# Optimization experiments

Hardware: AMD Instinct MI355X
Metric: run time of the kernel (lower is better)

The kernel has to match this reference:

```python
import jax, jax.numpy as jnp
import numpy as np

R = 8  # patch radius (init kwarg)


def setup_inputs() -> dict:
    key = jax.random.key(0)
    k1, k2, k3 = jax.random.split(key, 3)
    B, H, W, N = 8, 1024, 1024, 4096
    image1 = jax.random.normal(k1, (B, 1, H, W), dtype=jnp.float32)
    image2 = jax.random.normal(k2, (B, 1, H, W), dtype=jnp.float32)
    # (x1, y1, x2, y2) integer pixel coords in [0, H-1]
    matches = jax.random.randint(k3, (B, N, 4), 0, H, dtype=jnp.int32)
    return {"image1": image1, "image2": image2, "matches": matches}


def _normalize(p):
    # per-patch zero-mean / unit-std (unbiased std, matching torch.std)
    m = p.mean(axis=-1, keepdims=True)
    s = p.std(axis=-1, keepdims=True, ddof=1)
    return (p - m) / (s + 1e-4)


def reference(image1, image2, matches):
    r = R
    d = 2 * r + 1
    # offset grid, flattened row-major: lines[i,j]=i, columns[i,j]=j
    lines = jnp.repeat(jnp.arange(d, dtype=jnp.int32), d)   # [d^2]
    cols = jnp.tile(jnp.arange(d, dtype=jnp.int32), d)      # [d^2]
    # original M = [lines, columns, lines, columns]
    off = jnp.stack([lines, cols, lines, cols], axis=0)      # [4, d^2]
    idx = matches[..., None].astype(jnp.int32) + off          # [B, N, 4, d^2]

    def pad(im):  # [B,1,H,W] -> [B, H+2r, W+2r]
        return jnp.pad(im[:, 0], ((0, 0), (r, r), (r, r)))

    img1p, img2p = pad(image1), pad(image2)
    b = jnp.arange(matches.shape[0])[:, None, None]           # [B,1,1]
    # rows come from y-coord columns (1,3), cols from x-coord columns (0,2)
    p1 = img1p[b, idx[:, :, 1, :], idx[:, :, 0, :]]           # [B, N, d^2]
    p2 = img2p[b, idx[:, :, 3, :], idx[:, :, 2, :]]           # [B, N, d^2]
    return jnp.concatenate([_normalize(p1), _normalize(p2)], axis=-1)  # [B, N, 2*d^2]
```

## Files before the change

kernel.cpp:

```cpp
#include <hip/hip_runtime.h>
#include <hip/hip_bf16.h>


#define IMG_H 1024
#define IMG_W 1024
#define NMATCH 4096
#define DPATCH 17
#define NPATCH 289
#define RAD 8

__global__ __launch_bounds__(256) void prewarm_kernel(
    const float* __restrict__ img1,
    const float* __restrict__ img2)
{
    const int tid = blockIdx.x * blockDim.x + threadIdx.x;
    const int nthreads = gridDim.x * blockDim.x;
    const float4* __restrict__ a = (const float4*)img1;
    const float4* __restrict__ b = (const float4*)img2;
    const int n4 = (8 * IMG_H * IMG_W) / 4;
    float s = 0.f;
    for (int i = tid; i < n4; i += nthreads) {
        float4 x = a[i];
        float4 y = b[i];
        s += x.x + x.y + x.z + x.w + y.x + y.y + y.z + y.w;
    }
    asm volatile("" :: "v"(s));
}

__global__ __launch_bounds__(256) void extract_patch_kernel(
    const float* __restrict__ img1,
    const float* __restrict__ img2,
    const int* __restrict__ matches,
    float* __restrict__ out)
{
    __shared__ float smem[4 * NPATCH];

    const int tid  = blockIdx.x * blockDim.x + threadIdx.x;
    const int wave = tid >> 6;
    const int lane = tid & 63;
    const int pair  = wave >> 1;
    const int which = wave & 1;
    const int wbase = (threadIdx.x >> 6) * NPATCH;

    const int* m = matches + pair * 4;
    const int mx = m[which ? 2 : 0];
    const int my = m[which ? 3 : 1];

    const int b = pair >> 12;
    const float* __restrict__ imgb =
        (which ? img2 : img1) + (size_t)b * (IMG_H * IMG_W);

    const int g = lane / DPATCH;
    const int c = lane - g * DPATCH;
    const int ix = mx + c - RAD;
    const bool col_ok = (g < 3) && ((unsigned)ix < IMG_W);

    float sum = 0.f, sumsq = 0.f;
#pragma unroll
    for (int it = 0; it < 6; ++it) {
        const int r = it * 3 + g;
        float val = 0.f;
        if (g < 3 && r < DPATCH) {
            const int iy = my + r - RAD;
            if (col_ok && (unsigned)iy < IMG_H) {
                val = imgb[iy * IMG_W + ix];
            }
            smem[wbase + r + DPATCH * c] = val;
        }
        sum   += val;
        sumsq += val * val;
    }

#pragma unroll
    for (int off = 32; off > 0; off >>= 1) {
        sum   += __shfl_xor(sum,   off, 64);
        sumsq += __shfl_xor(sumsq, off, 64);
    }

    const float mean = sum * (1.0f / 289.0f);
    float var = (sumsq - 289.0f * mean * mean) * (1.0f / 288.0f);
    var = fmaxf(var, 0.0f);
    const float inv = 1.0f / (sqrtf(var) + 1e-4f);

    float* __restrict__ o = out + (size_t)pair * 578 + which * NPATCH;
#pragma unroll
    for (int k = 0; k < 5; ++k) {
        const int j = lane + (k << 6);
        if (j < NPATCH) {
            o[j] = (smem[wbase + j] - mean) * inv;
        }
    }
}

extern "C" void kernel_launch(void* const* d_in, const int* in_sizes, int n_in,
                              void* d_out, int out_size, void* d_ws, size_t ws_size,
                              hipStream_t stream) {
    const float* img1  = (const float*)d_in[0];
    const float* img2  = (const float*)d_in[1];
    const int* matches = (const int*)d_in[2];
    float* out         = (float*)d_out;

    hipLaunchKernelGGL(prewarm_kernel, dim3(2048), dim3(256), 0, stream,
                       img1, img2);

    const int n_waves = 8 * NMATCH * 2;
    dim3 block(256);
    dim3 grid(n_waves * 64 / 256);
    hipLaunchKernelGGL(extract_patch_kernel, grid, block, 0, stream,
                       img1, img2, matches, out);
}
```

Before: 155.6 us.

## Process four patches per wave with batched unconditional gathers and nontemporal stores

Each wave now handles two match pairs (four patches) instead of one patch, and issues all 24 gather loads up front with clamped addresses and select-based masking rather than branches. This raises memory-level parallelism per wave and amortizes the reductions and index math. Output writes use nontemporal stores to avoid polluting cache. The cost is a 4x smaller grid, more registers and 4x the LDS per block, which may reduce occupancy.

Result: no change. 153.3 us (-1.4%).

```diff
diff --git a/kernel.cpp b/kernel.cpp
--- a/kernel.cpp
+++ b/kernel.cpp
@@ -8,6 +8,7 @@
 #define DPATCH 17
 #define NPATCH 289
 #define RAD 8
+#define HW (IMG_H * IMG_W)
 
 __global__ __launch_bounds__(256) void prewarm_kernel(
     const float* __restrict__ img1,
@@ -17,7 +18,7 @@
     const int nthreads = gridDim.x * blockDim.x;
     const float4* __restrict__ a = (const float4*)img1;
     const float4* __restrict__ b = (const float4*)img2;
-    const int n4 = (8 * IMG_H * IMG_W) / 4;
+    const int n4 = (8 * HW) / 4;
     float s = 0.f;
     for (int i = tid; i < n4; i += nthreads) {
         float4 x = a[i];
@@ -33,61 +34,93 @@
     const int* __restrict__ matches,
     float* __restrict__ out)
 {
-    __shared__ float smem[4 * NPATCH];
+    __shared__ float smem[4 * 4 * NPATCH];
 
-    const int tid  = blockIdx.x * blockDim.x + threadIdx.x;
-    const int wave = tid >> 6;
-    const int lane = tid & 63;
-    const int pair  = wave >> 1;
-    const int which = wave & 1;
-    const int wbase = (threadIdx.x >> 6) * NPATCH;
-
-    const int* m = matches + pair * 4;
-    const int mx = m[which ? 2 : 0];
-    const int my = m[which ? 3 : 1];
-
-    const int b = pair >> 12;
-    const float* __restrict__ imgb =
-        (which ? img2 : img1) + (size_t)b * (IMG_H * IMG_W);
+    const int tid   = blockIdx.x * blockDim.x + threadIdx.x;
+    const int wave  = tid >> 6;
+    const int lane  = tid & 63;
+    const int wslot = threadIdx.x >> 6;
+    const int pair0 = wave << 1;
 
     const int g = lane / DPATCH;
     const int c = lane - g * DPATCH;
-    const int ix = mx + c - RAD;
-    const bool col_ok = (g < 3) && ((unsigned)ix < IMG_W);
+    const bool active = (g < 3);
 
-    float sum = 0.f, sumsq = 0.f;
+    const int b = pair0 >> 12;
+    const float* __restrict__ base1 = img1 + (size_t)b * HW;
+    const float* __restrict__ base2 = img2 + (size_t)b * HW;
+
+    int mx[4], my[4];
 #pragma unroll
-    for (int it = 0; it < 6; ++it) {
-        const int r = it * 3 + g;
-        float val = 0.f;
-        if (g < 3 && r < DPATCH) {
-            const int iy = my + r - RAD;
-            if (col_ok && (unsigned)iy < IMG_H) {
-                val = imgb[iy * IMG_W + ix];
-            }
-            smem[wbase + r + DPATCH * c] = val;
+    for (int t = 0; t < 4; ++t) {
+        const int pr = pair0 + (t >> 1);
+        const int wh = t & 1;
+        mx[t] = matches[pr * 4 + (wh ? 2 : 0)];
+        my[t] = matches[pr * 4 + (wh ? 3 : 1)];
+    }
+
+    float v[4][6];
+#pragma unroll
+    for (int t = 0; t < 4; ++t) {
+        const float* __restrict__ ib = (t & 1) ? base2 : base1;
+        const int ix = mx[t] + c - RAD;
+#pragma unroll
+        for (int it = 0; it < 6; ++it) {
+            const int r  = it * 3 + g;
+            const int iy = my[t] + r - RAD;
+            const bool ok = active && (r < DPATCH) &&
+                            ((unsigned)ix < IMG_W) && ((unsigned)iy < IMG_H);
+            const int off = ok ? (iy * IMG_W + ix) : 0;
+            const float val = ib[off];
+            v[t][it] = ok ? val : 0.f;
         }
-        sum   += val;
-        sumsq += val * val;
     }
 
 #pragma unroll
-    for (int off = 32; off > 0; off >>= 1) {
-        sum   += __shfl_xor(sum,   off, 64);
-        sumsq += __shfl_xor(sumsq, off, 64);
+    for (int t = 0; t < 4; ++t) {
+#pragma unroll
+        for (int it = 0; it < 6; ++it) {
+            const int r = it * 3 + g;
+            if (active && r < DPATCH) {
+                smem[(wslot * 4 + t) * NPATCH + r + DPATCH * c] = v[t][it];
+            }
+        }
     }
 
-    const float mean = sum * (1.0f / 289.0f);
-    float var = (sumsq - 289.0f * mean * mean) * (1.0f / 288.0f);
-    var = fmaxf(var, 0.0f);
-    const float inv = 1.0f / (sqrtf(var) + 1e-4f);
+    float s[4], q[4];
+#pragma unroll
+    for (int t = 0; t < 4; ++t) {
+        s[t] = 0.f; q[t] = 0.f;
+#pragma unroll
+        for (int it = 0; it < 6; ++it) {
+            s[t] += v[t][it];
+            q[t] += v[t][it] * v[t][it];
+        }
+    }
+#pragma unroll
+    for (int off = 32; off > 0; off >>= 1) {
+#pragma unroll
+        for (int t = 0; t < 4; ++t) {
+            s[t] += __shfl_xor(s[t], off, 64);
+            q[t] += __shfl_xor(q[t], off, 64);
+        }
+    }
 
-    float* __restrict__ o = out + (size_t)pair * 578 + which * NPATCH;
+    float* __restrict__ o0 = out + (size_t)pair0 * 578;
 #pragma unroll
-    for (int k = 0; k < 5; ++k) {
-        const int j = lane + (k << 6);
-        if (j < NPATCH) {
-            o[j] = (smem[wbase + j] - mean) * inv;
+    for (int t = 0; t < 4; ++t) {
+        const float mean = s[t] * (1.0f / 289.0f);
+        float var = (q[t] - 289.0f * mean * mean) * (1.0f / 288.0f);
+        var = fmaxf(var, 0.0f);
+        const float inv = 1.0f / (sqrtf(var) + 1e-4f);
+        float* __restrict__ o = o0 + t * NPATCH;
+#pragma unroll
+        for (int k = 0; k < 5; ++k) {
+            const int j = lane + (k << 6);
+            if (j < NPATCH) {
+                const float z = (smem[(wslot * 4 + t) * NPATCH + j] - mean) * inv;
+                __builtin_nontemporal_store(z, &o[j]);
+            }
         }
     }
 }
@@ -103,9 +136,6 @@
     hipLaunchKernelGGL(prewarm_kernel, dim3(2048), dim3(256), 0, stream,
                        img1, img2);
 
-    const int n_waves = 8 * NMATCH * 2;
-    dim3 block(256);
-    dim3 grid(n_waves * 64 / 256);
-    hipLaunchKernelGGL(extract_patch_kernel, grid, block, 0, stream,
+    hipLaunchKernelGGL(extract_patch_kernel, dim3(4096), dim3(256), 0, stream,
                        img1, img2, matches, out);
 }
```
